# Kernel tuning notes

Measured on AMD Instinct MI355X. Metric: run time of the kernel, lower is better.

## Reference

```python
import jax, jax.numpy as jnp
import numpy as np

B, H, W, C = 2, 256, 256, 96
HEADS, WS, K = 6, 16, 64
HID = C // 8          # MoE hidden (reduction=8)
MLP = 2 * C           # mlp_ratio=2
KS = 5                # convffn / lepe kernel
N = H * W
WSQ = WS * WS
HEAD_D = C // HEADS


def _dwconv(x, w, b, pad):
    # x: [B,C,H,W], w: [C,1,k,k] depthwise conv
    y = jax.lax.conv_general_dilated(x, w, (1, 1), [(pad, pad), (pad, pad)],
        dimension_numbers=('NCHW', 'OIHW', 'NCHW'), feature_group_count=x.shape[1])
    return y + b[None, :, None, None]


def _ln(x, g, b):
    mu = x.mean(-1, keepdims=True)
    var = ((x - mu) ** 2).mean(-1, keepdims=True)
    return (x - mu) * jax.lax.rsqrt(var + 1e-5) * g + b


def _gelu(x):
    return jax.nn.gelu(x, approximate=False)


def _lrelu(x):
    return jnp.where(x >= 0, x, 0.2 * x)


def _make_rpi():
    coords = np.stack(np.meshgrid(np.arange(WS), np.arange(WS), indexing='ij'))
    cf = coords.reshape(2, -1)
    rel = (cf[:, :, None] - cf[:, None, :]).transpose(1, 2, 0).astype(np.int32)
    rel[..., 0] += WS - 1
    rel[..., 1] += WS - 1
    rel[..., 0] *= 2 * WS - 1
    return jnp.asarray(rel.sum(-1))  # [WSQ, WSQ]


def setup_inputs():
    key = jax.random.key(0)
    ks = iter(jax.random.split(key, 64))
    nrm = lambda shape, s=0.02: jax.random.normal(next(ks), shape, jnp.float32) * s
    inp = {}
    inp['x'] = jax.random.normal(next(ks), (B, N, C), jnp.float32)
    inp['n1_g'] = jnp.ones((C,), jnp.float32); inp['n1_b'] = jnp.zeros((C,), jnp.float32)
    inp['n2_g'] = jnp.ones((C,), jnp.float32); inp['n2_b'] = jnp.zeros((C,), jnp.float32)
    inp['g_w1'] = nrm((HID, C)); inp['g_b1'] = jnp.zeros((HID,), jnp.float32)
    inp['g_w2'] = nrm((3, HID)); inp['g_b2'] = jnp.zeros((3,), jnp.float32)
    for i, k_sz in zip((1, 2, 3), (3, 5, 7)):
        inp[f'e{i}_w1'] = nrm((HID, C)); inp[f'e{i}_b1'] = jnp.zeros((HID,), jnp.float32)
        inp[f'e{i}_pw'] = nrm((HID, HID))
        inp[f'e{i}_dw'] = nrm((HID, 1, k_sz, k_sz), 0.1); inp[f'e{i}_dwb'] = jnp.zeros((HID,), jnp.float32)
        inp[f'e{i}_w2'] = nrm((C, HID)); inp[f'e{i}_b2'] = jnp.zeros((C,), jnp.float32)
    inp['moe_scale'] = jnp.full((1,), 0.001, jnp.float32)
    inp['qkv_w'] = nrm((3 * C, C)); inp['qkv_b'] = jnp.zeros((3 * C,), jnp.float32)
    inp['lepe_w'] = nrm((C, 1, KS, KS), 0.1); inp['lepe_b'] = jnp.zeros((C,), jnp.float32)
    inp['rpb'] = nrm(((2 * WS - 1) ** 2, HEADS))
    inp['proj_w'] = nrm((C, C)); inp['proj_b'] = jnp.zeros((C,), jnp.float32)
    inp['fc1_w'] = nrm((MLP, C)); inp['fc1_b'] = jnp.zeros((MLP,), jnp.float32)
    inp['ffn_dw'] = nrm((MLP, 1, KS, KS), 0.1); inp['ffn_db'] = jnp.zeros((MLP,), jnp.float32)
    inp['fc2_w'] = nrm((C, MLP)); inp['fc2_b'] = jnp.zeros((C,), jnp.float32)
    inp['rpi'] = _make_rpi()
    return inp


def _forward(x, n1_g, n1_b, n2_g, n2_b, g_w1, g_b1, g_w2, g_b2,
             e1_w1, e1_b1, e1_pw, e1_dw, e1_dwb, e1_w2, e1_b2,
             e2_w1, e2_b1, e2_pw, e2_dw, e2_dwb, e2_w2, e2_b2,
             e3_w1, e3_b1, e3_pw, e3_dw, e3_dwb, e3_w2, e3_b2,
             moe_scale, qkv_w, qkv_b, lepe_w, lepe_b, rpb, proj_w, proj_b,
             fc1_w, fc1_b, ffn_dw, ffn_db, fc2_w, fc2_b, rpi):
    b, n, c = x.shape
    shortcut = x
    y = _ln(x, n1_g, n1_b)
    img = y.reshape(b, H, W, c).transpose(0, 3, 1, 2)  # [b,c,H,W]

    # ---- MultiScaleMoEBlock ----
    pooled = img.mean((2, 3))                                   # [b,c]
    g = jax.nn.relu(pooled @ g_w1.T + g_b1)
    g = jax.nn.softmax(g @ g_w2.T + g_b2, axis=-1)              # [b,3]

    def expert(z, w1, b1, pw, dw, dwb, w2, b2, pad):
        t = _lrelu(jnp.einsum('bchw,oc->bohw', z, w1) + b1[None, :, None, None])
        t = jnp.einsum('bchw,oc->bohw', t, pw)                  # BSConvU pw (no bias)
        t = _lrelu(_dwconv(t, dw, dwb, pad))                    # BSConvU dw
        return jnp.einsum('bchw,oc->bohw', t, w2) + b2[None, :, None, None]

    o = (g[:, 0, None, None, None] * expert(img, e1_w1, e1_b1, e1_pw, e1_dw, e1_dwb, e1_w2, e1_b2, 1)
         + g[:, 1, None, None, None] * expert(img, e2_w1, e2_b1, e2_pw, e2_dw, e2_dwb, e2_w2, e2_b2, 2)
         + g[:, 2, None, None, None] * expert(img, e3_w1, e3_b1, e3_pw, e3_dw, e3_dwb, e3_w2, e3_b2, 3))
    img = img + o * moe_scale[0]
    y = img.transpose(0, 2, 3, 1).reshape(b, n, c)

    # ---- qkv + LePE ----
    qkv = y @ qkv_w.T + qkv_b                                   # [b,n,3c]
    v = qkv[..., 2 * c:]
    vimg = v.reshape(b, H, W, c).transpose(0, 3, 1, 2)
    lepe = _gelu(_dwconv(vimg, lepe_w, lepe_b, (KS - 1) // 2)).transpose(0, 2, 3, 1).reshape(b, n, c)
    xq = jnp.concatenate([qkv, lepe], -1).reshape(b, H, W, 4 * c)

    # ---- window partition (shift=0) ----
    win = xq.reshape(b, H // WS, WS, W // WS, WS, 4 * c).transpose(0, 1, 3, 2, 4, 5).reshape(-1, WSQ, 4 * c)
    Bw = win.shape[0]
    qkvl = win.reshape(Bw, WSQ, 4, HEADS, HEAD_D).transpose(2, 0, 3, 1, 4)
    q, k_, vv, lp = qkvl[0], qkvl[1], qkvl[2], qkvl[3]          # each [Bw,H,N,d]

    attn = jnp.einsum('bhnd,bhmd->bhnm', q * (HEAD_D ** -0.5), k_)
    bias = rpb[rpi].transpose(2, 0, 1)                          # [heads,WSQ,WSQ]
    attn = jax.nn.softmax(attn + bias[None], axis=-1)

    # top-k progressive focused attention (first layer: pfa is None)
    vals, idx = jax.lax.top_k(attn, K)                          # [Bw,heads,WSQ,K]
    bi = jnp.arange(Bw)[:, None, None, None]
    hi = jnp.arange(HEADS)[None, :, None, None]
    ni = jnp.arange(WSQ)[None, None, :, None]
    attn_s = jnp.zeros_like(attn).at[bi, hi, ni, idx].set(vals)
    out = jnp.einsum('bhnm,bhmd->bhnd', attn_s, vv) + lp
    out = out.transpose(0, 2, 1, 3).reshape(Bw, WSQ, c)
    out = out @ proj_w.T + proj_b

    # ---- window reverse ----
    out = out.reshape(b, H // WS, W // WS, WS, WS, c).transpose(0, 1, 3, 2, 4, 5).reshape(b, n, c)
    x = shortcut + out

    # ---- ConvFFN ----
    y = _ln(x, n2_g, n2_b)
    t = _gelu(y @ fc1_w.T + fc1_b)
    timg = t.reshape(b, H, W, MLP).transpose(0, 3, 1, 2)
    t = t + _gelu(_dwconv(timg, ffn_dw, ffn_db, (KS - 1) // 2)).transpose(0, 2, 3, 1).reshape(b, n, MLP)
    x = x + (t @ fc2_w.T + fc2_b)
    return x


def reference(x, n1_g, n1_b, n2_g, n2_b, g_w1, g_b1, g_w2, g_b2,
              e1_w1, e1_b1, e1_pw, e1_dw, e1_dwb, e1_w2, e1_b2,
              e2_w1, e2_b1, e2_pw, e2_dw, e2_dwb, e2_w2, e2_b2,
              e3_w1, e3_b1, e3_pw, e3_dw, e3_dwb, e3_w2, e3_b2,
              moe_scale, qkv_w, qkv_b, lepe_w, lepe_b, rpb, proj_w, proj_b,
              fc1_w, fc1_b, ffn_dw, ffn_db, fc2_w, fc2_b, rpi):
    return _forward(x, n1_g, n1_b, n2_g, n2_b, g_w1, g_b1, g_w2, g_b2,
                    e1_w1, e1_b1, e1_pw, e1_dw, e1_dwb, e1_w2, e1_b2,
                    e2_w1, e2_b1, e2_pw, e2_dw, e2_dwb, e2_w2, e2_b2,
                    e3_w1, e3_b1, e3_pw, e3_dw, e3_dwb, e3_w2, e3_b2,
                    moe_scale, qkv_w, qkv_b, lepe_w, lepe_b, rpb, proj_w, proj_b,
                    fc1_w, fc1_b, ffn_dw, ffn_db, fc2_w, fc2_b, rpi)
```

## Files before the change

kernel.cpp:

```cpp
#include <hip/hip_runtime.h>
#include <cstdint>

#define BB 2
#define HH_ 256
#define WW_ 256
#define CC 96
#define NTOK 65536
#define MTOK 131072
#define HEADS 6
#define WS 16
#define WSQ 256
#define HEAD_D 16
#define TOPK 64
#define HID 12
#define MLP_ 192

typedef short v8s __attribute__((ext_vector_type(8)));
typedef float v4f __attribute__((ext_vector_type(4)));

__device__ __forceinline__ float gelu_f(float v) {
  return 0.5f * v * (1.0f + erff(v * 0.70710678118654752440f));
}
__device__ __forceinline__ float lrelu_f(float v) { return v >= 0.0f ? v : 0.2f * v; }
__device__ __forceinline__ unsigned short bf16r(float f) {
  unsigned u = __float_as_uint(f);
  unsigned r = u + 0x7fffu + ((u >> 16) & 1u);
  return (unsigned short)(r >> 16);
}
__device__ __forceinline__ float bf16d(unsigned short h) {
  return __uint_as_float(((unsigned)h) << 16);
}

__global__ __launch_bounds__(256) void ln_kernel(const float* __restrict__ in,
    const float* __restrict__ gam, const float* __restrict__ bet, float* __restrict__ out) {
  int wid = blockIdx.x * 4 + (threadIdx.x >> 6);
  int lane = threadIdx.x & 63;
  const float* row = in + (size_t)wid * CC;
  float v0 = row[lane];
  float v1 = (lane < 32) ? row[64 + lane] : 0.0f;
  float s = v0 + v1;
  #pragma unroll
  for (int off = 32; off; off >>= 1) s += __shfl_xor(s, off);
  float mean = s * (1.0f / 96.0f);
  float d0 = v0 - mean;
  float d1 = (lane < 32) ? (v1 - mean) : 0.0f;
  float q = d0 * d0 + d1 * d1;
  #pragma unroll
  for (int off = 32; off; off >>= 1) q += __shfl_xor(q, off);
  float r = rsqrtf(q * (1.0f / 96.0f) + 1e-5f);
  float* orow = out + (size_t)wid * CC;
  orow[lane] = d0 * r * gam[lane] + bet[lane];
  if (lane < 32) orow[64 + lane] = d1 * r * gam[64 + lane] + bet[64 + lane];
}

__global__ __launch_bounds__(128) void pool_kernel(const float* __restrict__ A, float* __restrict__ pooled) {
  int c = threadIdx.x;
  if (c >= CC) return;
  int b = blockIdx.y;
  int t0 = blockIdx.x * 512;
  const float* base = A + ((size_t)b * NTOK + t0) * CC + c;
  float acc = 0.0f;
  #pragma unroll 8
  for (int t = 0; t < 512; t++) acc += base[(size_t)t * CC];
  atomicAdd(&pooled[b * CC + c], acc);
}

__global__ __launch_bounds__(64) void gate_kernel(const float* __restrict__ pooled,
    const float* __restrict__ w1, const float* __restrict__ b1,
    const float* __restrict__ w2, const float* __restrict__ b2, float* __restrict__ gv) {
  __shared__ float hb[BB][HID];
  __shared__ float lb[BB][3];
  int tid = threadIdx.x;
  if (tid < BB * HID) {
    int b = tid / HID, o = tid % HID;
    float s = b1[o];
    for (int c = 0; c < CC; c++) s += (pooled[b * CC + c] * (1.0f / 65536.0f)) * w1[o * CC + c];
    hb[b][o] = fmaxf(s, 0.0f);
  }
  __syncthreads();
  if (tid < BB * 3) {
    int b = tid / 3, j = tid % 3;
    float s = b2[j];
    for (int o = 0; o < HID; o++) s += hb[b][o] * w2[j * HID + o];
    lb[b][j] = s;
  }
  __syncthreads();
  if (tid < BB) {
    float m = fmaxf(lb[tid][0], fmaxf(lb[tid][1], lb[tid][2]));
    float e0 = __expf(lb[tid][0] - m), e1 = __expf(lb[tid][1] - m), e2 = __expf(lb[tid][2] - m);
    float inv = 1.0f / (e0 + e1 + e2);
    gv[tid * 3 + 0] = e0 * inv; gv[tid * 3 + 1] = e1 * inv; gv[tid * 3 + 2] = e2 * inv;
  }
}

template <int K, int NO, int ACT, bool RESID, bool HASB>
__global__ __launch_bounds__(256, 4) void mgemm_kernel(const float* __restrict__ A,
    const float* __restrict__ W, const float* __restrict__ bias,
    const float* __restrict__ resid, float* __restrict__ out, int ostride, int rstride) {
  __shared__ __align__(16) unsigned short al[128][104];
  __shared__ __align__(16) unsigned short wl[64][104];
  int tid = threadIdx.x;
  int lane = tid & 63, wv = tid >> 6, quad = lane >> 4, to = lane & 15;
  int o0 = blockIdx.x * 64, p0 = blockIdx.y * 128;
  v4f acc[2][4];
  #pragma unroll
  for (int ni = 0; ni < 4; ni++) {
    float bv = 0.0f;
    if (HASB) { int o = o0 + ni * 16 + to; if (o < NO) bv = bias[o]; }
    #pragma unroll
    for (int mi = 0; mi < 2; mi++) acc[mi][ni] = (v4f){bv, bv, bv, bv};
  }
  for (int kc = 0; kc < K; kc += 96) {
    __syncthreads();
    {
      int r = tid & 127, half = tid >> 7;
      const float* ap = A + (size_t)(p0 + r) * K + kc + half * 48;
      #pragma unroll
      for (int g = 0; g < 3; g++) {
        float4 f0 = *(const float4*)(ap + g * 16);
        float4 f1 = *(const float4*)(ap + g * 16 + 4);
        float4 f2 = *(const float4*)(ap + g * 16 + 8);
        float4 f3 = *(const float4*)(ap + g * 16 + 12);
        uint4 u, v;
        u.x = (unsigned)bf16r(f0.x) | ((unsigned)bf16r(f0.y) << 16);
        u.y = (unsigned)bf16r(f0.z) | ((unsigned)bf16r(f0.w) << 16);
        u.z = (unsigned)bf16r(f1.x) | ((unsigned)bf16r(f1.y) << 16);
        u.w = (unsigned)bf16r(f1.z) | ((unsigned)bf16r(f1.w) << 16);
        v.x = (unsigned)bf16r(f2.x) | ((unsigned)bf16r(f2.y) << 16);
        v.y = (unsigned)bf16r(f2.z) | ((unsigned)bf16r(f2.w) << 16);
        v.z = (unsigned)bf16r(f3.x) | ((unsigned)bf16r(f3.y) << 16);
        v.w = (unsigned)bf16r(f3.z) | ((unsigned)bf16r(f3.w) << 16);
        *(uint4*)&al[r][half * 48 + g * 16] = u;
        *(uint4*)&al[r][half * 48 + g * 16 + 8] = v;
      }
    }
    {
      int r = tid & 63, q = tid >> 6;
      int o = o0 + r;
      if (o < NO) {
        const float* wp = W + (size_t)o * K + kc + q * 24;
        #pragma unroll
        for (int g = 0; g < 3; g++) {
          float4 f0 = *(const float4*)(wp + g * 8);
          float4 f1 = *(const float4*)(wp + g * 8 + 4);
          uint4 u;
          u.x = (unsigned)bf16r(f0.x) | ((unsigned)bf16r(f0.y) << 16);
          u.y = (unsigned)bf16r(f0.z) | ((unsigned)bf16r(f0.w) << 16);
          u.z = (unsigned)bf16r(f1.x) | ((unsigned)bf16r(f1.y) << 16);
          u.w = (unsigned)bf16r(f1.z) | ((unsigned)bf16r(f1.w) << 16);
          *(uint4*)&wl[r][q * 24 + g * 8] = u;
        }
      } else {
        uint4 z = make_uint4(0, 0, 0, 0);
        #pragma unroll
        for (int g = 0; g < 3; g++) *(uint4*)&wl[r][q * 24 + g * 8] = z;
      }
    }
    __syncthreads();
    #pragma unroll
    for (int ks = 0; ks < 3; ks++) {
      v8s af[2], bfr[4];
      #pragma unroll
      for (int mi = 0; mi < 2; mi++)
        af[mi] = *(const v8s*)&al[wv * 32 + mi * 16 + to][ks * 32 + quad * 8];
      #pragma unroll
      for (int ni = 0; ni < 4; ni++)
        bfr[ni] = *(const v8s*)&wl[ni * 16 + to][ks * 32 + quad * 8];
      #pragma unroll
      for (int mi = 0; mi < 2; mi++)
        #pragma unroll
        for (int ni = 0; ni < 4; ni++)
          acc[mi][ni] = __builtin_amdgcn_mfma_f32_16x16x32_bf16(af[mi], bfr[ni], acc[mi][ni], 0, 0, 0);
    }
  }
  #pragma unroll
  for (int mi = 0; mi < 2; mi++)
    #pragma unroll
    for (int ni = 0; ni < 4; ni++) {
      int o = o0 + ni * 16 + to;
      if (o < NO) {
        #pragma unroll
        for (int rg = 0; rg < 4; rg++) {
          int p = p0 + wv * 32 + mi * 16 + quad * 4 + rg;
          float v = acc[mi][ni][rg];
          if (ACT == 1) v = lrelu_f(v);
          else if (ACT == 2) v = gelu_f(v);
          if (RESID) v += resid[(size_t)p * rstride + o];
          out[(size_t)p * ostride + o] = v;
        }
      }
    }
}

template <int K, int KC, int NO, int ACT, bool RESID, bool HASB>
__global__ __launch_bounds__(256) void gemm_kernel(const float* __restrict__ in,
    const float* __restrict__ w, const float* __restrict__ bias,
    const float* __restrict__ resid, float* __restrict__ out, int ostride, int rstride) {
  __shared__ __align__(16) float xs[64][KC + 4];
  __shared__ __align__(16) float ws[64][KC + 4];
  int tid = threadIdx.x;
  int p0 = blockIdx.x * 64;
  int o0 = blockIdx.y * 64;
  int to = tid & 15, tp = tid >> 4;
  float acc[4][4];
  #pragma unroll
  for (int j = 0; j < 4; j++) {
    float bv = 0.0f;
    if (HASB) { int o = o0 + to + 16 * j; if (o < NO) bv = bias[o]; }
    #pragma unroll
    for (int i = 0; i < 4; i++) acc[i][j] = bv;
  }
  for (int kc = 0; kc < K; kc += KC) {
    __syncthreads();
    for (int idx = tid; idx < 64 * (KC / 4); idx += 256) {
      int p = idx / (KC / 4), c4 = idx % (KC / 4);
      *(float4*)&xs[p][c4 * 4] = *(const float4*)&in[(size_t)(p0 + p) * K + kc + c4 * 4];
    }
    for (int idx = tid; idx < 64 * (KC / 4); idx += 256) {
      int r = idx / (KC / 4), c4 = idx % (KC / 4);
      int o = o0 + r;
      float4 v = make_float4(0.f, 0.f, 0.f, 0.f);
      if (o < NO) v = *(const float4*)&w[(size_t)o * K + kc + c4 * 4];
      *(float4*)&ws[r][c4 * 4] = v;
    }
    __syncthreads();
    #pragma unroll 4
    for (int cc = 0; cc < KC; cc += 4) {
      float4 xv[4], wv[4];
      #pragma unroll
      for (int i = 0; i < 4; i++) xv[i] = *(const float4*)&xs[tp + 16 * i][cc];
      #pragma unroll
      for (int j = 0; j < 4; j++) wv[j] = *(const float4*)&ws[to + 16 * j][cc];
      #pragma unroll
      for (int i = 0; i < 4; i++)
        #pragma unroll
        for (int j = 0; j < 4; j++)
          acc[i][j] += xv[i].x * wv[j].x + xv[i].y * wv[j].y + xv[i].z * wv[j].z + xv[i].w * wv[j].w;
    }
  }
  #pragma unroll
  for (int i = 0; i < 4; i++) {
    int p = p0 + tp + 16 * i;
    #pragma unroll
    for (int j = 0; j < 4; j++) {
      int o = o0 + to + 16 * j;
      if (o < NO) {
        float v = acc[i][j];
        if (ACT == 1) v = lrelu_f(v);
        else if (ACT == 2) v = gelu_f(v);
        if (RESID) v += resid[(size_t)p * rstride + o];
        out[(size_t)p * ostride + o] = v;
      }
    }
  }
}

template <int KSZ, int CH, int ACT, bool RESID>
__global__ __launch_bounds__(256) void dwconv_kernel(const float* __restrict__ in,
    const float* __restrict__ wt, const float* __restrict__ wb,
    const float* __restrict__ resid, float* __restrict__ out,
    int istride, int ostride, int rstride) {
  constexpr int C4 = CH / 4;
  constexpr int K2 = KSZ * KSZ;
  int e = blockIdx.x * 256 + threadIdx.x;
  int c4 = e % C4;
  int pix = e / C4;
  int b = pix >> 16, n = pix & 65535, h = n >> 8, w = n & 255;
  const int P = (KSZ - 1) / 2;
  int c = c4 * 4;
  float4 acc = *(const float4*)(wb + c);
  #pragma unroll
  for (int ky = 0; ky < KSZ; ky++) {
    int hh = h + ky - P;
    if (hh < 0 || hh >= HH_) continue;
    #pragma unroll
    for (int kx = 0; kx < KSZ; kx++) {
      int ww = w + kx - P;
      if (ww < 0 || ww >= WW_) continue;
      float4 iv = *(const float4*)(in + ((size_t)(b << 16) + (hh << 8) + ww) * istride + c);
      int t = ky * KSZ + kx;
      acc.x += wt[(c + 0) * K2 + t] * iv.x;
      acc.y += wt[(c + 1) * K2 + t] * iv.y;
      acc.z += wt[(c + 2) * K2 + t] * iv.z;
      acc.w += wt[(c + 3) * K2 + t] * iv.w;
    }
  }
  if (ACT == 1) {
    acc.x = lrelu_f(acc.x); acc.y = lrelu_f(acc.y); acc.z = lrelu_f(acc.z); acc.w = lrelu_f(acc.w);
  } else if (ACT == 2) {
    acc.x = gelu_f(acc.x); acc.y = gelu_f(acc.y); acc.z = gelu_f(acc.z); acc.w = gelu_f(acc.w);
  }
  if (RESID) {
    float4 rv = *(const float4*)(resid + (size_t)pix * rstride + c);
    acc.x += rv.x; acc.y += rv.y; acc.z += rv.z; acc.w += rv.w;
  }
  *(float4*)(out + (size_t)pix * ostride + c) = acc;
}

template <int KSZ, int CH, int ACT, bool RESID>
__global__ __launch_bounds__(256) void dwconv4_kernel(const float* __restrict__ in,
    const float* __restrict__ wt, const float* __restrict__ wb,
    const float* __restrict__ resid, float* __restrict__ out,
    int istride, int ostride, int rstride) {
  constexpr int C4 = CH / 4;
  constexpr int K2 = KSZ * KSZ;
  constexpr int P = (KSZ - 1) / 2;
  constexpr int NC = KSZ + 3;
  int e = blockIdx.x * 256 + threadIdx.x;
  int c4 = e % C4;
  int g = e / C4;
  int b = g >> 14, rem = g & 16383, h = rem >> 6, w0 = (rem & 63) << 2;
  int c = c4 * 4;
  float4 wbv = *(const float4*)(wb + c);
  float4 acc[4] = {wbv, wbv, wbv, wbv};
  #pragma unroll
  for (int ky = 0; ky < KSZ; ky++) {
    int hh = h + ky - P;
    if (hh < 0 || hh >= HH_) continue;
    const float* rowp = in + ((size_t)(b << 16) + (hh << 8)) * istride + c;
    float4 iv[NC];
    #pragma unroll
    for (int k = 0; k < NC; k++) {
      int ww = w0 - P + k;
      if (ww >= 0 && ww < WW_) iv[k] = *(const float4*)(rowp + (size_t)ww * istride);
      else iv[k] = make_float4(0.f, 0.f, 0.f, 0.f);
    }
    #pragma unroll
    for (int kx = 0; kx < KSZ; kx++) {
      int t = ky * KSZ + kx;
      float wt0 = wt[(c + 0) * K2 + t];
      float wt1 = wt[(c + 1) * K2 + t];
      float wt2 = wt[(c + 2) * K2 + t];
      float wt3 = wt[(c + 3) * K2 + t];
      #pragma unroll
      for (int px = 0; px < 4; px++) {
        acc[px].x += wt0 * iv[kx + px].x;
        acc[px].y += wt1 * iv[kx + px].y;
        acc[px].z += wt2 * iv[kx + px].z;
        acc[px].w += wt3 * iv[kx + px].w;
      }
    }
  }
  #pragma unroll
  for (int px = 0; px < 4; px++) {
    float4 a = acc[px];
    if (ACT == 1) {
      a.x = lrelu_f(a.x); a.y = lrelu_f(a.y); a.z = lrelu_f(a.z); a.w = lrelu_f(a.w);
    } else if (ACT == 2) {
      a.x = gelu_f(a.x); a.y = gelu_f(a.y); a.z = gelu_f(a.z); a.w = gelu_f(a.w);
    }
    size_t pix = (size_t)(b << 16) + (h << 8) + w0 + px;
    if (RESID) {
      float4 rv = *(const float4*)(resid + pix * rstride + c);
      a.x += rv.x; a.y += rv.y; a.z += rv.z; a.w += rv.w;
    }
    *(float4*)(out + pix * ostride + c) = a;
  }
}

__global__ __launch_bounds__(256) void moe_combine_kernel(float* __restrict__ A,
    const float* __restrict__ t3a, const float* __restrict__ t3b, const float* __restrict__ t3c,
    const float* __restrict__ w2a, const float* __restrict__ w2b, const float* __restrict__ w2c,
    const float* __restrict__ b2a, const float* __restrict__ b2b, const float* __restrict__ b2c,
    const float* __restrict__ gv, const float* __restrict__ ms) {
  int e4 = blockIdx.x * 256 + threadIdx.x;
  int c4 = e4 % (CC / 4), pix = e4 / (CC / 4), b = pix >> 16;
  int c = c4 * 4;
  float4 sa = *(const float4*)(b2a + c);
  float4 sb = *(const float4*)(b2b + c);
  float4 sc = *(const float4*)(b2c + c);
  #pragma unroll
  for (int h2 = 0; h2 < HID; h2++) {
    float ta = t3a[(size_t)pix * HID + h2];
    float tb = t3b[(size_t)pix * HID + h2];
    float tc = t3c[(size_t)pix * HID + h2];
    sa.x += ta * w2a[(c + 0) * HID + h2]; sa.y += ta * w2a[(c + 1) * HID + h2];
    sa.z += ta * w2a[(c + 2) * HID + h2]; sa.w += ta * w2a[(c + 3) * HID + h2];
    sb.x += tb * w2b[(c + 0) * HID + h2]; sb.y += tb * w2b[(c + 1) * HID + h2];
    sb.z += tb * w2b[(c + 2) * HID + h2]; sb.w += tb * w2b[(c + 3) * HID + h2];
    sc.x += tc * w2c[(c + 0) * HID + h2]; sc.y += tc * w2c[(c + 1) * HID + h2];
    sc.z += tc * w2c[(c + 2) * HID + h2]; sc.w += tc * w2c[(c + 3) * HID + h2];
  }
  float g0 = gv[b * 3 + 0], g1 = gv[b * 3 + 1], g2 = gv[b * 3 + 2], m0 = ms[0];
  float* ap = A + (size_t)pix * CC + c;
  float4 av = *(const float4*)ap;
  av.x += m0 * (g0 * sa.x + g1 * sb.x + g2 * sc.x);
  av.y += m0 * (g0 * sa.y + g1 * sb.y + g2 * sc.y);
  av.z += m0 * (g0 * sa.z + g1 * sb.z + g2 * sc.z);
  av.w += m0 * (g0 * sa.w + g1 * sb.w + g2 * sc.w);
  *(float4*)ap = av;
}

__global__ __launch_bounds__(256) void bias_kernel(const int* __restrict__ rpi,
    const float* __restrict__ rpb, float* __restrict__ biasT) {
  int idx = blockIdx.x * 256 + threadIdx.x;
  int h = idx >> 16, nm = idx & 65535;
  int n = nm >> 8, m = nm & 255;
  biasT[(h << 16) + ((n >> 2) << 10) + (m << 2) + (n & 3)] = rpb[rpi[nm] * HEADS + h];
}

__global__ __launch_bounds__(256, 3) void attn_kernel(const float* __restrict__ X,
    const float* __restrict__ biasT, float* __restrict__ O) {
  __shared__ __align__(16) unsigned short kb[256][16];
  __shared__ __align__(16) unsigned short vt[16][264];
  __shared__ __align__(16) unsigned short sSb[2][16][264];
  int tid = threadIdx.x;
  int wi = blockIdx.x, hh = blockIdx.y;
  int b = wi >> 8, wrem = wi & 255, wy = wrem >> 4, wx = wrem & 15;
  int lane = tid & 63, wv_ = tid >> 6, quad = lane >> 4, to = lane & 15;

  {
    int m = tid;
    int nm = (((wy << 4) + (m >> 4)) << 8) | ((wx << 4) + (m & 15));
    size_t xb = ((size_t)(b << 16) + nm) * 288 + hh * 16;
    float kr[16], vr[16];
    *(float4*)&kr[0]  = *(const float4*)(X + xb + 96);
    *(float4*)&kr[4]  = *(const float4*)(X + xb + 100);
    *(float4*)&kr[8]  = *(const float4*)(X + xb + 104);
    *(float4*)&kr[12] = *(const float4*)(X + xb + 108);
    *(float4*)&vr[0]  = *(const float4*)(X + xb + 192);
    *(float4*)&vr[4]  = *(const float4*)(X + xb + 196);
    *(float4*)&vr[8]  = *(const float4*)(X + xb + 200);
    *(float4*)&vr[12] = *(const float4*)(X + xb + 204);
    unsigned u_[8];
    #pragma unroll
    for (int i = 0; i < 8; i++)
      u_[i] = (unsigned)bf16r(kr[2 * i]) | ((unsigned)bf16r(kr[2 * i + 1]) << 16);
    *(uint4*)&kb[m][0] = make_uint4(u_[0], u_[1], u_[2], u_[3]);
    *(uint4*)&kb[m][8] = make_uint4(u_[4], u_[5], u_[6], u_[7]);
    #pragma unroll
    for (int d = 0; d < 16; d++) vt[d][m] = bf16r(vr[d]);
  }

  auto load_q = [&](int ch) -> v8s {
    v8s af = {0, 0, 0, 0, 0, 0, 0, 0};
    if (quad < 2) {
      int nq = (((wy << 4) + ch) << 8) | ((wx << 4) + to);
      const float* qp = X + ((size_t)(b << 16) + nq) * 288 + hh * 16 + quad * 8;
      float4 f0 = *(const float4*)qp;
      float4 f1 = *(const float4*)(qp + 4);
      uint4 u;
      u.x = (unsigned)bf16r(f0.x * 0.25f) | ((unsigned)bf16r(f0.y * 0.25f) << 16);
      u.y = (unsigned)bf16r(f0.z * 0.25f) | ((unsigned)bf16r(f0.w * 0.25f) << 16);
      u.z = (unsigned)bf16r(f1.x * 0.25f) | ((unsigned)bf16r(f1.y * 0.25f) << 16);
      u.w = (unsigned)bf16r(f1.z * 0.25f) | ((unsigned)bf16r(f1.w * 0.25f) << 16);
      af = *(v8s*)&u;
    }
    return af;
  };

  v8s afc = load_q(0);
  __syncthreads();

  #pragma unroll 1
  for (int i = 0; i < 16; i++) {
    unsigned short (*sw)[264] = sSb[i & 1];
    int r0 = i * 16;
    bool avw = (wv_ == (i & 3));
    size_t ob = 0;
    float oc0 = 0.f, oc1 = 0.f, oc2 = 0.f, oc3 = 0.f;
    if (avw) {
      int n_o = (((wy << 4) + i) << 8) | ((wx << 4) + (quad << 2));
      ob = ((size_t)(b << 16) + n_o) * CC + hh * 16 + to;
      oc0 = O[ob]; oc1 = O[ob + 96]; oc2 = O[ob + 192]; oc3 = O[ob + 288];
    }
    #pragma unroll
    for (int t = 0; t < 4; t++) {
      int c0 = (wv_ * 4 + t) * 16;
      v8s bfr = {0, 0, 0, 0, 0, 0, 0, 0};
      if (quad < 2) bfr = *(const v8s*)&kb[c0 + to][quad * 8];
      float4 bv = *(const float4*)(biasT + ((size_t)hh << 16) +
                                   (size_t)(((r0 >> 2) + quad) << 10) + ((c0 + to) << 2));
      v4f cf;
      cf[0] = bv.x; cf[1] = bv.y; cf[2] = bv.z; cf[3] = bv.w;
      cf = __builtin_amdgcn_mfma_f32_16x16x32_bf16(afc, bfr, cf, 0, 0, 0);
      #pragma unroll
      for (int rg = 0; rg < 4; rg++)
        sw[quad * 4 + rg][c0 + to] = (unsigned short)(__float_as_uint(cf[rg]) >> 16);
    }
    if (i < 15) afc = load_q(i + 1);
    __syncthreads();
    {
      float ex_[4][4], inv_[4];
      unsigned uk[4][4], cand[4];
      int hb[4]; bool done[4];
      #pragma unroll
      for (int qr = 0; qr < 4; qr++) {
        int r = wv_ * 4 + qr;
        unsigned h0 = sw[r][lane], h1 = sw[r][64 + lane];
        unsigned h2 = sw[r][128 + lane], h3 = sw[r][192 + lane];
        float x0 = __uint_as_float(h0 << 16), x1 = __uint_as_float(h1 << 16);
        float x2 = __uint_as_float(h2 << 16), x3 = __uint_as_float(h3 << 16);
        float mx = fmaxf(fmaxf(x0, x1), fmaxf(x2, x3));
        #pragma unroll
        for (int off = 32; off; off >>= 1) mx = fmaxf(mx, __shfl_xor(mx, off));
        float e0 = __expf(x0 - mx), e1 = __expf(x1 - mx), e2 = __expf(x2 - mx), e3 = __expf(x3 - mx);
        float sm = e0 + e1 + e2 + e3;
        #pragma unroll
        for (int off = 32; off; off >>= 1) sm += __shfl_xor(sm, off);
        inv_[qr] = 1.0f / sm;
        ex_[qr][0] = e0; ex_[qr][1] = e1; ex_[qr][2] = e2; ex_[qr][3] = e3;
        unsigned u0 = (h0 & 0x8000u) ? (h0 ^ 0xFFFFu) : (h0 | 0x8000u);
        unsigned u1 = (h1 & 0x8000u) ? (h1 ^ 0xFFFFu) : (h1 | 0x8000u);
        unsigned u2 = (h2 & 0x8000u) ? (h2 ^ 0xFFFFu) : (h2 | 0x8000u);
        unsigned u3 = (h3 & 0x8000u) ? (h3 ^ 0xFFFFu) : (h3 | 0x8000u);
        uk[qr][0] = u0; uk[qr][1] = u1; uk[qr][2] = u2; uk[qr][3] = u3;
        unsigned ad = u0 & u1 & u2 & u3;
        unsigned orr = u0 | u1 | u2 | u3;
        #pragma unroll
        for (int off = 32; off; off >>= 1) {
          ad &= __shfl_xor(ad, off);
          orr |= __shfl_xor(orr, off);
        }
        unsigned diff = ad ^ orr;
        hb[qr] = diff ? (31 - __builtin_clz(diff)) : -1;
        unsigned lowmask = (hb[qr] < 0) ? 0u : ((1u << (hb[qr] + 1)) - 1u);
        cand[qr] = ad & ~lowmask;
        done[qr] = (hb[qr] < 0);
      }
      int hbmax = max(max(hb[0], hb[1]), max(hb[2], hb[3]));
      for (int bit = hbmax; bit >= 0; --bit) {
        if (done[0] && done[1] && done[2] && done[3]) break;
        #pragma unroll
        for (int qr = 0; qr < 4; qr++) {
          if (done[qr] || bit > hb[qr]) continue;
          unsigned t = cand[qr] | (1u << bit);
          int cnt = __popcll(__ballot(uk[qr][0] >= t)) + __popcll(__ballot(uk[qr][1] >= t)) +
                    __popcll(__ballot(uk[qr][2] >= t)) + __popcll(__ballot(uk[qr][3] >= t));
          if (cnt >= TOPK) { cand[qr] = t; if (cnt == TOPK) done[qr] = true; }
        }
      }
      #pragma unroll
      for (int qr = 0; qr < 4; qr++) {
        int r = wv_ * 4 + qr;
        unsigned c_ = cand[qr];
        int gcnt = __popcll(__ballot(uk[qr][0] > c_)) + __popcll(__ballot(uk[qr][1] > c_)) +
                   __popcll(__ballot(uk[qr][2] > c_)) + __popcll(__ballot(uk[qr][3] > c_));
        int need = TOPK - gcnt;
        unsigned long long q0 = __ballot(uk[qr][0] == c_), q1 = __ballot(uk[qr][1] == c_);
        unsigned long long q2 = __ballot(uk[qr][2] == c_), q3 = __ballot(uk[qr][3] == c_);
        unsigned long long lt = ((unsigned long long)1 << lane) - 1ull;
        int p0c = __popcll(q0 & lt);
        int p1c = __popcll(q0) + __popcll(q1 & lt);
        int p2c = __popcll(q0) + __popcll(q1) + __popcll(q2 & lt);
        int p3c = __popcll(q0) + __popcll(q1) + __popcll(q2) + __popcll(q3 & lt);
        float iv = inv_[qr];
        sw[r][lane]       = (uk[qr][0] > c_ || (uk[qr][0] == c_ && p0c < need)) ? bf16r(ex_[qr][0] * iv) : (unsigned short)0;
        sw[r][64 + lane]  = (uk[qr][1] > c_ || (uk[qr][1] == c_ && p1c < need)) ? bf16r(ex_[qr][1] * iv) : (unsigned short)0;
        sw[r][128 + lane] = (uk[qr][2] > c_ || (uk[qr][2] == c_ && p2c < need)) ? bf16r(ex_[qr][2] * iv) : (unsigned short)0;
        sw[r][192 + lane] = (uk[qr][3] > c_ || (uk[qr][3] == c_ && p3c < need)) ? bf16r(ex_[qr][3] * iv) : (unsigned short)0;
      }
    }
    __syncthreads();
    if (avw) {
      v4f acc = {0.f, 0.f, 0.f, 0.f};
      #pragma unroll
      for (int kc = 0; kc < 8; kc++) {
        v8s paf = *(const v8s*)&sw[to][kc * 32 + quad * 8];
        v8s vbf = *(const v8s*)&vt[to][kc * 32 + quad * 8];
        acc = __builtin_amdgcn_mfma_f32_16x16x32_bf16(paf, vbf, acc, 0, 0, 0);
      }
      O[ob]       = oc0 + acc[0];
      O[ob + 96]  = oc1 + acc[1];
      O[ob + 192] = oc2 + acc[2];
      O[ob + 288] = oc3 + acc[3];
    }
  }
}

extern "C" void kernel_launch(void* const* d_in, const int* in_sizes, int n_in,
                              void* d_out, int out_size, void* d_ws, size_t ws_size,
                              hipStream_t stream) {
  (void)in_sizes; (void)n_in; (void)out_size; (void)ws_size;
  const float* x     = (const float*)d_in[0];
  const float* n1_g  = (const float*)d_in[1];
  const float* n1_b  = (const float*)d_in[2];
  const float* n2_g  = (const float*)d_in[3];
  const float* n2_b  = (const float*)d_in[4];
  const float* g_w1  = (const float*)d_in[5];
  const float* g_b1  = (const float*)d_in[6];
  const float* g_w2  = (const float*)d_in[7];
  const float* g_b2  = (const float*)d_in[8];
  const float* e_w1[3]  = {(const float*)d_in[9],  (const float*)d_in[16], (const float*)d_in[23]};
  const float* e_b1[3]  = {(const float*)d_in[10], (const float*)d_in[17], (const float*)d_in[24]};
  const float* e_pw[3]  = {(const float*)d_in[11], (const float*)d_in[18], (const float*)d_in[25]};
  const float* e_dw[3]  = {(const float*)d_in[12], (const float*)d_in[19], (const float*)d_in[26]};
  const float* e_dwb[3] = {(const float*)d_in[13], (const float*)d_in[20], (const float*)d_in[27]};
  const float* e_w2[3]  = {(const float*)d_in[14], (const float*)d_in[21], (const float*)d_in[28]};
  const float* e_b2[3]  = {(const float*)d_in[15], (const float*)d_in[22], (const float*)d_in[29]};
  const float* ms    = (const float*)d_in[30];
  const float* qkv_w = (const float*)d_in[31];
  const float* qkv_b = (const float*)d_in[32];
  const float* lepe_w = (const float*)d_in[33];
  const float* lepe_b = (const float*)d_in[34];
  const float* rpb   = (const float*)d_in[35];
  const float* proj_w = (const float*)d_in[36];
  const float* proj_b = (const float*)d_in[37];
  const float* fc1_w = (const float*)d_in[38];
  const float* fc1_b = (const float*)d_in[39];
  const float* ffn_dw = (const float*)d_in[40];
  const float* ffn_db = (const float*)d_in[41];
  const float* fc2_w = (const float*)d_in[42];
  const float* fc2_b = (const float*)d_in[43];
  const int*   rpi   = (const int*)d_in[44];
  float* out = (float*)d_out;

  const size_t M = MTOK;
  float* ws = (float*)d_ws;
  float* A   = ws;
  float* t1  = ws + 96 * M;
  float* t2b = ws + 108 * M;
  float* t3[3] = { ws + 120 * M, ws + 132 * M, ws + 144 * M };
  float* X   = ws + 96 * M;
  float* T   = ws + 192 * M;
  float* T2  = ws;
  float* O   = A;
  float* S2  = out;
  float* biasT = out;
  float* pooled = ws + 384 * M;
  float* gv = pooled + 192;

  bias_kernel<<<HEADS * NTOK / 256, 256, 0, stream>>>(rpi, rpb, biasT);
  ln_kernel<<<M / 4, 256, 0, stream>>>(x, n1_g, n1_b, A);
  hipMemsetAsync(pooled, 0, 256 * sizeof(float), stream);
  pool_kernel<<<dim3(128, 2), 128, 0, stream>>>(A, pooled);
  gate_kernel<<<1, 64, 0, stream>>>(pooled, g_w1, g_b1, g_w2, g_b2, gv);
  for (int i = 0; i < 3; i++) {
    mgemm_kernel<96, 12, 1, false, true><<<dim3(1, 1024), 256, 0, stream>>>(
        A, e_w1[i], e_b1[i], nullptr, t1, 12, 0);
    gemm_kernel<12, 12, 12, 0, false, false><<<dim3(2048, 1), 256, 0, stream>>>(
        t1, e_pw[i], nullptr, nullptr, t2b, 12, 0);
    if (i == 0)
      dwconv_kernel<3, 12, 1, false><<<M * 3 / 256, 256, 0, stream>>>(t2b, e_dw[0], e_dwb[0], nullptr, t3[0], 12, 12, 0);
    else if (i == 1)
      dwconv_kernel<5, 12, 1, false><<<M * 3 / 256, 256, 0, stream>>>(t2b, e_dw[1], e_dwb[1], nullptr, t3[1], 12, 12, 0);
    else
      dwconv_kernel<7, 12, 1, false><<<M * 3 / 256, 256, 0, stream>>>(t2b, e_dw[2], e_dwb[2], nullptr, t3[2], 12, 12, 0);
  }
  moe_combine_kernel<<<M * 24 / 256, 256, 0, stream>>>(A,
      t3[0], t3[1], t3[2], e_w2[0], e_w2[1], e_w2[2], e_b2[0], e_b2[1], e_b2[2], gv, ms);
  mgemm_kernel<96, 288, 0, false, true><<<dim3(5, 1024), 256, 0, stream>>>(
      A, qkv_w, qkv_b, nullptr, X, 288, 0);
  dwconv4_kernel<5, 96, 2, false><<<M * 6 / 256, 256, 0, stream>>>(X + 192, lepe_w, lepe_b, nullptr, O, 288, 96, 0);
  attn_kernel<<<dim3(512, 6), 256, 0, stream>>>(X, biasT, O);
  mgemm_kernel<96, 96, 0, true, true><<<dim3(2, 1024), 256, 0, stream>>>(
      O, proj_w, proj_b, x, S2, 96, 96);
  ln_kernel<<<M / 4, 256, 0, stream>>>(S2, n2_g, n2_b, A);
  mgemm_kernel<96, 192, 2, false, true><<<dim3(3, 1024), 256, 0, stream>>>(
      A, fc1_w, fc1_b, nullptr, T, 192, 0);
  dwconv4_kernel<5, 192, 2, true><<<M * 12 / 256, 256, 0, stream>>>(T, ffn_dw, ffn_db, T, T2, 192, 192, 192);
  mgemm_kernel<192, 96, 0, true, true><<<dim3(2, 1024), 256, 0, stream>>>(
      T2, fc2_w, fc2_b, S2, out, 96, 96);
}
```

Before: 1.705 ms.

## Split attention query chunks across two wave groups with 512-thread blocks

The attention kernel now launches 512 threads per block, organised as two groups of four waves. Each group handles alternating 16-query chunks with its own double-buffered score tile in shared memory, which halves the serial chunk loop from 16 to 8 iterations. The intent is more parallelism per window and more latency hiding across the top-k selection. In exchange, shared memory per block roughly doubles and block-wide barriers now span eight waves, which may lower occupancy.

Result: slower. 1.751 ms (+2.7%).

```diff
diff --git a/kernel.cpp b/kernel.cpp
--- a/kernel.cpp
+++ b/kernel.cpp
@@ -399,17 +399,18 @@
   biasT[(h << 16) + ((n >> 2) << 10) + (m << 2) + (n & 3)] = rpb[rpi[nm] * HEADS + h];
 }
 
-__global__ __launch_bounds__(256, 3) void attn_kernel(const float* __restrict__ X,
+__global__ __launch_bounds__(512, 3) void attn_kernel(const float* __restrict__ X,
     const float* __restrict__ biasT, float* __restrict__ O) {
   __shared__ __align__(16) unsigned short kb[256][16];
   __shared__ __align__(16) unsigned short vt[16][264];
-  __shared__ __align__(16) unsigned short sSb[2][16][264];
+  __shared__ __align__(16) unsigned short sSb[2][2][16][264];
   int tid = threadIdx.x;
   int wi = blockIdx.x, hh = blockIdx.y;
   int b = wi >> 8, wrem = wi & 255, wy = wrem >> 4, wx = wrem & 15;
   int lane = tid & 63, wv_ = tid >> 6, quad = lane >> 4, to = lane & 15;
-
-  {
+  int wg = wv_ >> 2, wl = wv_ & 3;
+
+  if (tid < 256) {
     int m = tid;
     int nm = (((wy << 4) + (m >> 4)) << 8) | ((wx << 4) + (m & 15));
     size_t xb = ((size_t)(b << 16) + nm) * 288 + hh * 16;
@@ -449,24 +450,25 @@
     return af;
   };
 
-  v8s afc = load_q(0);
+  v8s afc = load_q(wg);
   __syncthreads();
 
   #pragma unroll 1
-  for (int i = 0; i < 16; i++) {
-    unsigned short (*sw)[264] = sSb[i & 1];
-    int r0 = i * 16;
-    bool avw = (wv_ == (i & 3));
+  for (int t = 0; t < 8; t++) {
+    int ch = 2 * t + wg;
+    unsigned short (*sw)[264] = sSb[wg][t & 1];
+    int r0 = ch * 16;
+    bool avw = (wl == (t & 3));
     size_t ob = 0;
     float oc0 = 0.f, oc1 = 0.f, oc2 = 0.f, oc3 = 0.f;
     if (avw) {
-      int n_o = (((wy << 4) + i) << 8) | ((wx << 4) + (quad << 2));
+      int n_o = (((wy << 4) + ch) << 8) | ((wx << 4) + (quad << 2));
       ob = ((size_t)(b << 16) + n_o) * CC + hh * 16 + to;
       oc0 = O[ob]; oc1 = O[ob + 96]; oc2 = O[ob + 192]; oc3 = O[ob + 288];
     }
     #pragma unroll
-    for (int t = 0; t < 4; t++) {
-      int c0 = (wv_ * 4 + t) * 16;
+    for (int tt = 0; tt < 4; tt++) {
+      int c0 = (wl * 4 + tt) * 16;
       v8s bfr = {0, 0, 0, 0, 0, 0, 0, 0};
       if (quad < 2) bfr = *(const v8s*)&kb[c0 + to][quad * 8];
       float4 bv = *(const float4*)(biasT + ((size_t)hh << 16) +
@@ -478,7 +480,7 @@
       for (int rg = 0; rg < 4; rg++)
         sw[quad * 4 + rg][c0 + to] = (unsigned short)(__float_as_uint(cf[rg]) >> 16);
     }
-    if (i < 15) afc = load_q(i + 1);
+    if (t < 7) afc = load_q(ch + 2);
     __syncthreads();
     {
       float ex_[4][4], inv_[4];
@@ -486,7 +488,7 @@
       int hb[4]; bool done[4];
       #pragma unroll
       for (int qr = 0; qr < 4; qr++) {
-        int r = wv_ * 4 + qr;
+        int r = wl * 4 + qr;
         unsigned h0 = sw[r][lane], h1 = sw[r][64 + lane];
         unsigned h2 = sw[r][128 + lane], h3 = sw[r][192 + lane];
         float x0 = __uint_as_float(h0 << 16), x1 = __uint_as_float(h1 << 16);
@@ -524,15 +526,15 @@
         #pragma unroll
         for (int qr = 0; qr < 4; qr++) {
           if (done[qr] || bit > hb[qr]) continue;
-          unsigned t = cand[qr] | (1u << bit);
-          int cnt = __popcll(__ballot(uk[qr][0] >= t)) + __popcll(__ballot(uk[qr][1] >= t)) +
-                    __popcll(__ballot(uk[qr][2] >= t)) + __popcll(__ballot(uk[qr][3] >= t));
-          if (cnt >= TOPK) { cand[qr] = t; if (cnt == TOPK) done[qr] = true; }
+          unsigned t2 = cand[qr] | (1u << bit);
+          int cnt = __popcll(__ballot(uk[qr][0] >= t2)) + __popcll(__ballot(uk[qr][1] >= t2)) +
+                    __popcll(__ballot(uk[qr][2] >= t2)) + __popcll(__ballot(uk[qr][3] >= t2));
+          if (cnt >= TOPK) { cand[qr] = t2; if (cnt == TOPK) done[qr] = true; }
         }
       }
       #pragma unroll
       for (int qr = 0; qr < 4; qr++) {
-        int r = wv_ * 4 + qr;
+        int r = wl * 4 + qr;
         unsigned c_ = cand[qr];
         int gcnt = __popcll(__ballot(uk[qr][0] > c_)) + __popcll(__ballot(uk[qr][1] > c_)) +
                    __popcll(__ballot(uk[qr][2] > c_)) + __popcll(__ballot(uk[qr][3] > c_));
@@ -642,7 +644,7 @@
   mgemm_kernel<96, 288, 0, false, true><<<dim3(5, 1024), 256, 0, stream>>>(
       A, qkv_w, qkv_b, nullptr, X, 288, 0);
   dwconv4_kernel<5, 96, 2, false><<<M * 6 / 256, 256, 0, stream>>>(X + 192, lepe_w, lepe_b, nullptr, O, 288, 96, 0);
-  attn_kernel<<<dim3(512, 6), 256, 0, stream>>>(X, biasT, O);
+  attn_kernel<<<dim3(512, 6), 512, 0, stream>>>(X, biasT, O);
   mgemm_kernel<96, 96, 0, true, true><<<dim3(2, 1024), 256, 0, stream>>>(
       O, proj_w, proj_b, x, S2, 96, 96);
   ln_kernel<<<M / 4, 256, 0, stream>>>(S2, n2_g, n2_b, A);
```
